# Optimization experiments

Measured on AMD Instinct MI355X. Metric: run time of the kernel, lower is better.

Reference implementation:

```python
import jax, jax.numpy as jnp
import numpy as np
from jax import lax

EPS = 1e-10
BN_EPS = 1e-5
T = 0.1
K = 64
B, D, H, Z = 2048, 2048, 512, 500


def _bn(x, g, b):
    # training-mode BatchNorm1d: biased batch stats over axis 0
    mu = x.mean(axis=0)
    var = ((x - mu) ** 2).mean(axis=0)
    return g * (x - mu) / jnp.sqrt(var + BN_EPS) + b


def _leaky(x):
    return jnp.where(x >= 0, x, 0.01 * x)


def setup_inputs() -> dict:
    key = jax.random.key(0)
    ks = jax.random.split(key, 16)
    def lin(k, fan_in, shape):
        return jax.random.normal(k, shape, jnp.float32) / np.sqrt(fan_in)
    return {
        'x': jax.random.uniform(ks[0], (B, D), jnp.float32),
        'u_gumbel': jax.random.uniform(ks[1], (B, D), jnp.float32),
        'eps': jax.random.normal(ks[2], (B, Z), jnp.float32),
        'wc_w1': lin(ks[3], D, (D, H)), 'wc_b1': jnp.zeros((H,)),
        'wc_g': jnp.ones((H,)), 'wc_beta': jnp.zeros((H,)),
        'wc_w2': lin(ks[4], H, (H, D)), 'wc_b2': jnp.zeros((D,)),
        'enc_w1': lin(ks[5], D, (D, 2 * H)), 'enc_b1': jnp.zeros((2 * H,)),
        'enc_g1': jnp.ones((2 * H,)), 'enc_beta1': jnp.zeros((2 * H,)),
        'enc_w2': lin(ks[6], 2 * H, (2 * H, H)), 'enc_b2': jnp.zeros((H,)),
        'enc_g2': jnp.ones((H,)), 'enc_beta2': jnp.zeros((H,)),
        'enc_w3': lin(ks[7], H, (H, H)), 'enc_b3': jnp.zeros((H,)),
        'enc_g3': jnp.ones((H,)), 'enc_beta3': jnp.zeros((H,)),
        'fc21_w': lin(ks[8], H, (H, Z)), 'fc21_b': jnp.zeros((Z,)),
        'fc22_w': lin(ks[9], H, (H, Z)), 'fc22_b': jnp.zeros((Z,)),
        'fc3_w': lin(ks[10], Z, (Z, H)), 'fc3_b': jnp.zeros((H,)),
        'fc3_g': jnp.ones((H,)), 'fc3_beta': jnp.zeros((H,)),
        'fc4_w': lin(ks[11], H, (H, D)), 'fc4_b': jnp.zeros((D,)),
    }


def _sample_subset(w_logits, u):
    # gumbel_keys: w += log(-log(u')) with u' in (EPS, 1)
    u = (1.0 - EPS) * u + EPS
    w = w_logits + jnp.log(-jnp.log(u))

    def step(carry, _):
        w, onehot, acc = carry
        khot_mask = jnp.maximum(1.0 - onehot, EPS)
        w = w + jnp.log(khot_mask)
        onehot = jax.nn.softmax(w / T, axis=-1)
        return (w, onehot, acc + onehot), None

    init = (w, jnp.zeros_like(w), jnp.zeros_like(w))
    (_, _, khot), _ = lax.scan(step, init, None, length=K)
    return khot


def reference(x, u_gumbel, eps,
              wc_w1, wc_b1, wc_g, wc_beta, wc_w2, wc_b2,
              enc_w1, enc_b1, enc_g1, enc_beta1,
              enc_w2, enc_b2, enc_g2, enc_beta2,
              enc_w3, enc_b3, enc_g3, enc_beta3,
              fc21_w, fc21_b, fc22_w, fc22_b,
              fc3_w, fc3_b, fc3_g, fc3_beta, fc4_w, fc4_b):
    # weight_creator: Linear -> BN -> ReLU -> Linear
    h = jax.nn.relu(_bn(x @ wc_w1 + wc_b1, wc_g, wc_beta))
    w_logits = h @ wc_w2 + wc_b2
    khot = _sample_subset(w_logits, u_gumbel)  # [B, D]
    xm = x * khot
    h1 = _leaky(_bn(xm @ enc_w1 + enc_b1, enc_g1, enc_beta1))
    h1 = _leaky(_bn(h1 @ enc_w2 + enc_b2, enc_g2, enc_beta2))
    h1 = _leaky(_bn(h1 @ enc_w3 + enc_b3, enc_g3, enc_beta3))
    mu = h1 @ fc21_w + fc21_b
    logvar = h1 @ fc22_w + fc22_b
    z = mu + eps * jnp.exp(0.5 * logvar)
    hd = _leaky(_bn(z @ fc3_w + fc3_b, fc3_g, fc3_beta))
    mu_x = jax.nn.sigmoid(hd @ fc4_w + fc4_b)
    return (mu_x, mu, logvar)
```

## Files before the change

kernel.cpp:

```cpp
#include <hip/hip_runtime.h>
#include <hip/hip_bf16.h>
#include <math.h>

#define B_DIM 2048
#define D_DIM 2048
#define H_DIM 512
#define Z_DIM 500

#define ACT_NONE 0
#define ACT_RELU 1
#define ACT_SIGMOID 2
#define ACT_LEAKY 3

typedef __attribute__((ext_vector_type(8))) _Float16 f16x8;
typedef __attribute__((ext_vector_type(4))) _Float16 f16x4;
typedef __attribute__((ext_vector_type(4))) float f32x4;

struct HL { _Float16 h, l; };
__device__ __forceinline__ HL split_f16(float a) {
    HL r;
    r.h = (_Float16)a;
    r.l = (_Float16)(a - (float)r.h);
    return r;
}

template<int TERMS>
__global__ __launch_bounds__(256, 2) void gemm_k(
    const float* __restrict__ A, const float* __restrict__ W,
    const float* __restrict__ bias, float* __restrict__ C,
    float* __restrict__ part, int M, int N, int K, int act, int Kc)
{
    constexpr int BM = 64, BN = 64, LDK = 40;
    constexpr int PS = BM * LDK;
    constexpr int NP = (TERMS == 3) ? 4 : 2;
    __shared__ _Float16 smem[2 * NP * PS];

    const int t = threadIdx.x;
    const int lane = t & 63;
    const int wv = t >> 6;
    const int wrow = wv >> 1, wcol = wv & 1;
    const int row0 = blockIdx.y * BM, col0 = blockIdx.x * BN;
    const int s = blockIdx.z;
    const int ks = s * Kc;
    const int ke = min(ks + Kc, K);
    const int nk = (ke > ks) ? ((ke - ks + 31) >> 5) : 0;

    const int ar = t >> 3;
    const int ako = (t & 7) << 2;
    const int bn_ = t & 63;
    const int bks = (t >> 6) << 3;
    const int gn = col0 + bn_;

    float4 aR[2];
    float bR[8];

    auto gload = [&](int kt) {
        int gk = kt + ako;
        #pragma unroll
        for (int p = 0; p < 2; ++p) {
            const float* ap = A + (size_t)(row0 + p * 32 + ar) * K + gk;
            float4 v = make_float4(0.f, 0.f, 0.f, 0.f);
            if (gk + 3 < ke) {
                v = *(const float4*)ap;
            } else {
                if (gk     < ke) v.x = ap[0];
                if (gk + 1 < ke) v.y = ap[1];
                if (gk + 2 < ke) v.z = ap[2];
                if (gk + 3 < ke) v.w = ap[3];
            }
            aR[p] = v;
        }
        #pragma unroll
        for (int i = 0; i < 8; ++i) {
            int gk2 = kt + bks + i;
            bR[i] = (gk2 < ke && gn < N) ? W[(size_t)gk2 * N + gn] : 0.f;
        }
    };

    auto cstore = [&](int b) {
        _Float16* Ah = smem + b * NP * PS;
        _Float16* Al = Ah + PS;
        _Float16* Bh = Ah + ((TERMS == 3) ? 2 : 1) * PS;
        _Float16* Bl = Bh + PS;
        #pragma unroll
        for (int p = 0; p < 2; ++p) {
            int r = p * 32 + ar;
            float4 v = aR[p];
            if constexpr (TERMS == 3) {
                HL s0 = split_f16(v.x), s1 = split_f16(v.y);
                HL s2 = split_f16(v.z), s3 = split_f16(v.w);
                f16x4 h4 = {s0.h, s1.h, s2.h, s3.h};
                f16x4 l4 = {s0.l, s1.l, s2.l, s3.l};
                *(f16x4*)&Ah[r * LDK + ako] = h4;
                *(f16x4*)&Al[r * LDK + ako] = l4;
            } else {
                f16x4 h4 = {(_Float16)v.x, (_Float16)v.y, (_Float16)v.z, (_Float16)v.w};
                *(f16x4*)&Ah[r * LDK + ako] = h4;
            }
        }
        if constexpr (TERMS == 3) {
            f16x8 h8, l8;
            #pragma unroll
            for (int i = 0; i < 8; ++i) { HL sp = split_f16(bR[i]); h8[i] = sp.h; l8[i] = sp.l; }
            *(f16x8*)&Bh[bn_ * LDK + bks] = h8;
            *(f16x8*)&Bl[bn_ * LDK + bks] = l8;
        } else {
            f16x8 h8;
            #pragma unroll
            for (int i = 0; i < 8; ++i) h8[i] = (_Float16)bR[i];
            *(f16x8*)&Bh[bn_ * LDK + bks] = h8;
        }
    };

    f32x4 acc[2][2];
    #pragma unroll
    for (int i = 0; i < 2; ++i)
        #pragma unroll
        for (int j = 0; j < 2; ++j) {
            f32x4 z = {0.f, 0.f, 0.f, 0.f};
            acc[i][j] = z;
        }

    const int q8 = (lane >> 4) * 8;
    const int fr = lane & 15;

    gload(ks);
    cstore(0);
    __syncthreads();

    for (int it = 0; it < nk; ++it) {
        int cur = it & 1;
        if (it + 1 < nk) gload(ks + (it + 1) * 32);

        {
            const _Float16* Ah = smem + cur * NP * PS;
            const _Float16* Al = Ah + PS;
            const _Float16* Bh = Ah + ((TERMS == 3) ? 2 : 1) * PS;
            const _Float16* Bl = Bh + PS;
            f16x8 ah[2], al[2], bh[2], bl[2];
            #pragma unroll
            for (int i = 0; i < 2; ++i) {
                int r = wrow * 32 + i * 16 + fr;
                ah[i] = *(const f16x8*)&Ah[r * LDK + q8];
                if constexpr (TERMS == 3) al[i] = *(const f16x8*)&Al[r * LDK + q8];
            }
            #pragma unroll
            for (int j = 0; j < 2; ++j) {
                int n = wcol * 32 + j * 16 + fr;
                bh[j] = *(const f16x8*)&Bh[n * LDK + q8];
                if constexpr (TERMS == 3) bl[j] = *(const f16x8*)&Bl[n * LDK + q8];
            }
            #pragma unroll
            for (int i = 0; i < 2; ++i)
                #pragma unroll
                for (int j = 0; j < 2; ++j) {
                    acc[i][j] = __builtin_amdgcn_mfma_f32_16x16x32_f16(ah[i], bh[j], acc[i][j], 0, 0, 0);
                    if constexpr (TERMS == 3) {
                        acc[i][j] = __builtin_amdgcn_mfma_f32_16x16x32_f16(ah[i], bl[j], acc[i][j], 0, 0, 0);
                        acc[i][j] = __builtin_amdgcn_mfma_f32_16x16x32_f16(al[i], bh[j], acc[i][j], 0, 0, 0);
                    }
                }
        }

        if (it + 1 < nk) cstore(cur ^ 1);
        __syncthreads();
    }

    const bool dopart = (gridDim.z > 1);
    float* dst = dopart ? (part + (size_t)s * M * N) : C;
    #pragma unroll
    for (int i = 0; i < 2; ++i) {
        int rbase = row0 + wrow * 32 + i * 16 + (lane >> 4) * 4;
        #pragma unroll
        for (int j = 0; j < 2; ++j) {
            int c = col0 + wcol * 32 + j * 16 + (lane & 15);
            if (c < N) {
                float b = dopart ? 0.f : bias[c];
                #pragma unroll
                for (int q = 0; q < 4; ++q) {
                    float v = acc[i][j][q] + b;
                    if (!dopart && act == ACT_SIGMOID)
                        v = 1.f / (1.f + __builtin_amdgcn_exp2f(-v * 1.44269504f));
                    dst[(size_t)(rbase + q) * N + c] = v;
                }
            }
        }
    }
}

__global__ __launch_bounds__(256) void reduce_bias(
    const float* __restrict__ part, int S, int MN, int N,
    const float* __restrict__ bias, float* __restrict__ C)
{
    int i = blockIdx.x * 256 + threadIdx.x;
    if (i >= MN) return;
    float s = bias[i % N];
    for (int k = 0; k < S; ++k) s += part[(size_t)k * MN + i];
    C[i] = s;
}

__global__ __launch_bounds__(256) void colstats_partial(
    const float* __restrict__ Y, float* __restrict__ part,
    int Brows, int N, int rowsPerBlock)
{
    const int t = threadIdx.x;
    const int col = blockIdx.x * 64 + (t & 63);
    const int g = blockIdx.y;
    const int r0 = g * rowsPerBlock;
    const int r1 = min(r0 + rowsPerBlock, Brows);
    float s = 0.f, s2 = 0.f;
    for (int r = r0 + (t >> 6); r < r1; r += 4) {
        float v = Y[(size_t)r * N + col];
        s += v;
        s2 += v * v;
    }
    __shared__ float ss[4][64], ss2[4][64];
    ss[t >> 6][t & 63] = s;
    ss2[t >> 6][t & 63] = s2;
    __syncthreads();
    if (t < 64) {
        s  = ss[0][t] + ss[1][t] + ss[2][t] + ss[3][t];
        s2 = ss2[0][t] + ss2[1][t] + ss2[2][t] + ss2[3][t];
        float* p = part + ((size_t)g * N + col) * 2;
        p[0] = s;
        p[1] = s2;
    }
}

__global__ __launch_bounds__(256) void colstats_final(
    const float* __restrict__ part, int G, int N, int Brows,
    const float* __restrict__ gamma, const float* __restrict__ beta,
    float* __restrict__ scale, float* __restrict__ shift)
{
    int c = blockIdx.x * 256 + threadIdx.x;
    if (c >= N) return;
    float s = 0.f, s2 = 0.f;
    for (int g = 0; g < G; ++g) {
        s  += part[((size_t)g * N + c) * 2];
        s2 += part[((size_t)g * N + c) * 2 + 1];
    }
    float invB = 1.f / (float)Brows;
    float mean = s * invB;
    float var  = s2 * invB - mean * mean;
    float rstd = rsqrtf(var + 1e-5f);
    float sc = gamma[c] * rstd;
    scale[c] = sc;
    shift[c] = beta[c] - mean * sc;
}

__global__ __launch_bounds__(256) void bn_apply(
    const float* __restrict__ Y, const float* __restrict__ scale,
    const float* __restrict__ shift, float* __restrict__ out,
    int total, int N, int act)
{
    int i4 = (blockIdx.x * 256 + threadIdx.x) * 4;
    if (i4 >= total) return;
    float4 y = *(const float4*)(Y + i4);
    int c = i4 % N;
    float4 sc = *(const float4*)(scale + c);
    float4 sh = *(const float4*)(shift + c);
    float4 r;
    r.x = y.x * sc.x + sh.x;
    r.y = y.y * sc.y + sh.y;
    r.z = y.z * sc.z + sh.z;
    r.w = y.w * sc.w + sh.w;
    if (act == ACT_RELU) {
        r.x = fmaxf(r.x, 0.f); r.y = fmaxf(r.y, 0.f);
        r.z = fmaxf(r.z, 0.f); r.w = fmaxf(r.w, 0.f);
    } else if (act == ACT_LEAKY) {
        r.x = (r.x >= 0.f) ? r.x : 0.01f * r.x;
        r.y = (r.y >= 0.f) ? r.y : 0.01f * r.y;
        r.z = (r.z >= 0.f) ? r.z : 0.01f * r.z;
        r.w = (r.w >= 0.f) ? r.w : 0.01f * r.w;
    }
    *(float4*)(out + i4) = r;
}

__global__ __launch_bounds__(256) void gumbel_scan_kernel(
    float* __restrict__ WL, const float* __restrict__ U,
    const float* __restrict__ X)
{
    const int row = blockIdx.x;
    const int t = threadIdx.x;
    const int wv = t >> 6;
    const int lane = t & 63;
    float* wrow = WL + (size_t)row * D_DIM;
    const float* urow = U + (size_t)row * D_DIM;
    const float* xrow = X + (size_t)row * D_DIM;

    const float L2E = 1.4426950408889634f;
    const float LOG2LN2 = -0.5287663729448977f;
    const float C10 = 10.0f;

    __shared__ float smax[4], ssum[4];

    float w2[8], oh[8], acc[8];
    #pragma unroll
    for (int j = 0; j < 8; ++j) {
        int c = t + j * 256;
        float u = urow[c];
        u = (1.0f - 1e-10f) * u + 1e-10f;
        float tl = -__builtin_amdgcn_logf(u);
        w2[j] = fmaf(wrow[c], L2E, __builtin_amdgcn_logf(tl) + LOG2LN2);
        oh[j] = 0.f;
        acc[j] = 0.f;
    }

    for (int it = 0; it < 64; ++it) {
        float m = -INFINITY;
        #pragma unroll
        for (int j = 0; j < 8; ++j) {
            float mask = fmaxf(1.0f - oh[j], 1e-10f);
            w2[j] += __builtin_amdgcn_logf(mask);
            m = fmaxf(m, w2[j]);
        }
        #pragma unroll
        for (int off = 32; off; off >>= 1)
            m = fmaxf(m, __shfl_xor(m, off));
        if (lane == 0) smax[wv] = m;
        __syncthreads();
        m = fmaxf(fmaxf(smax[0], smax[1]), fmaxf(smax[2], smax[3]));
        float mc = m * C10;
        float s = 0.f;
        #pragma unroll
        for (int j = 0; j < 8; ++j) {
            float e = __builtin_amdgcn_exp2f(fmaf(w2[j], C10, -mc));
            oh[j] = e;
            s += e;
        }
        #pragma unroll
        for (int off = 32; off; off >>= 1)
            s += __shfl_xor(s, off);
        if (lane == 0) ssum[wv] = s;
        __syncthreads();
        s = (ssum[0] + ssum[1]) + (ssum[2] + ssum[3]);
        float inv = 1.0f / s;
        #pragma unroll
        for (int j = 0; j < 8; ++j) {
            oh[j] *= inv;
            acc[j] += oh[j];
        }
    }

    #pragma unroll
    for (int j = 0; j < 8; ++j) {
        int c = t + j * 256;
        wrow[c] = xrow[c] * acc[j];
    }
}

__global__ __launch_bounds__(256) void z_kernel(
    const float* __restrict__ mu, const float* __restrict__ lv,
    const float* __restrict__ eps, float* __restrict__ z, int n4)
{
    int i = blockIdx.x * 256 + threadIdx.x;
    if (i >= n4) return;
    float4 m = ((const float4*)mu)[i];
    float4 l = ((const float4*)lv)[i];
    float4 e = ((const float4*)eps)[i];
    const float HL2E = 0.7213475204444817f;
    float4 r;
    r.x = m.x + e.x * __builtin_amdgcn_exp2f(l.x * HL2E);
    r.y = m.y + e.y * __builtin_amdgcn_exp2f(l.y * HL2E);
    r.z = m.z + e.z * __builtin_amdgcn_exp2f(l.z * HL2E);
    r.w = m.w + e.w * __builtin_amdgcn_exp2f(l.w * HL2E);
    ((float4*)z)[i] = r;
}

extern "C" void kernel_launch(void* const* d_in, const int* in_sizes, int n_in,
                              void* d_out, int out_size, void* d_ws, size_t ws_size,
                              hipStream_t stream) {
    const float* x        = (const float*)d_in[0];
    const float* u_gumbel = (const float*)d_in[1];
    const float* eps      = (const float*)d_in[2];
    const float* wc_w1    = (const float*)d_in[3];
    const float* wc_b1    = (const float*)d_in[4];
    const float* wc_g     = (const float*)d_in[5];
    const float* wc_beta  = (const float*)d_in[6];
    const float* wc_w2    = (const float*)d_in[7];
    const float* wc_b2    = (const float*)d_in[8];
    const float* enc_w1   = (const float*)d_in[9];
    const float* enc_b1   = (const float*)d_in[10];
    const float* enc_g1   = (const float*)d_in[11];
    const float* enc_beta1= (const float*)d_in[12];
    const float* enc_w2   = (const float*)d_in[13];
    const float* enc_b2   = (const float*)d_in[14];
    const float* enc_g2   = (const float*)d_in[15];
    const float* enc_beta2= (const float*)d_in[16];
    const float* enc_w3   = (const float*)d_in[17];
    const float* enc_b3   = (const float*)d_in[18];
    const float* enc_g3   = (const float*)d_in[19];
    const float* enc_beta3= (const float*)d_in[20];
    const float* fc21_w   = (const float*)d_in[21];
    const float* fc21_b   = (const float*)d_in[22];
    const float* fc22_w   = (const float*)d_in[23];
    const float* fc22_b   = (const float*)d_in[24];
    const float* fc3_w    = (const float*)d_in[25];
    const float* fc3_b    = (const float*)d_in[26];
    const float* fc3_g    = (const float*)d_in[27];
    const float* fc3_beta = (const float*)d_in[28];
    const float* fc4_w    = (const float*)d_in[29];
    const float* fc4_b    = (const float*)d_in[30];

    float* out   = (float*)d_out;
    float* mu_x  = out;
    float* mu    = out + (size_t)B_DIM * D_DIM;
    float* lv    = mu + (size_t)B_DIM * Z_DIM;

    const size_t M1 = 1048576;
    float* wsf   = (float*)d_ws;
    float* WL    = wsf;
    float* P     = wsf + 4 * M1;
    float* Hbuf  = wsf + 8 * M1;
    float* bnp   = wsf + 9 * M1;
    float* scale = bnp + 16384;
    float* shift = scale + 2048;

    float* Y2 = WL;
    float* Y3 = WL + 2 * M1;
    float* Y4 = WL + 3 * M1;
    float* Zb = WL;
    float* Y5 = WL + 1 * M1;

    const int G = 8;

    auto gemm = [&](int TERMS, const float* A, const float* W, const float* b,
                    float* C, float* part, int M, int N, int K, int act, int SK) {
        int Kc = ((K / SK + 31) / 32) * 32;
        dim3 grid((N + 63) / 64, M / 64, SK);
        if (TERMS == 3)
            gemm_k<3><<<grid, 256, 0, stream>>>(A, W, b, C, part, M, N, K, act, Kc);
        else
            gemm_k<1><<<grid, 256, 0, stream>>>(A, W, b, C, part, M, N, K, act, Kc);
    };
    auto reduceK = [&](const float* part, int S, int MN, int N, const float* b, float* C) {
        reduce_bias<<<(MN + 255) / 256, 256, 0, stream>>>(part, S, MN, N, b, C);
    };
    auto bn = [&](float* Y, const float* g_, const float* b_, int N, int act) {
        dim3 gp(N / 64, G);
        colstats_partial<<<gp, 256, 0, stream>>>(Y, bnp, B_DIM, N, B_DIM / G);
        colstats_final<<<(N + 255) / 256, 256, 0, stream>>>(bnp, G, N, B_DIM, g_, b_, scale, shift);
        int total = B_DIM * N;
        bn_apply<<<(total / 4 + 255) / 256, 256, 0, stream>>>(Y, scale, shift, Y, total, N, act);
    };

    gemm(3, x, wc_w1, nullptr, nullptr, P, B_DIM, H_DIM, D_DIM, ACT_NONE, 4);
    reduceK(P, 4, B_DIM * H_DIM, H_DIM, wc_b1, Hbuf);
    bn(Hbuf, wc_g, wc_beta, H_DIM, ACT_RELU);
    gemm(3, Hbuf, wc_w2, wc_b2, WL, nullptr, B_DIM, D_DIM, H_DIM, ACT_NONE, 1);

    gumbel_scan_kernel<<<B_DIM, 256, 0, stream>>>(WL, u_gumbel, x);

    gemm(1, WL, enc_w1, nullptr, nullptr, P, B_DIM, 2 * H_DIM, D_DIM, ACT_NONE, 2);
    reduceK(P, 2, B_DIM * 2 * H_DIM, 2 * H_DIM, enc_b1, Y2);
    bn(Y2, enc_g1, enc_beta1, 2 * H_DIM, ACT_LEAKY);
    gemm(1, Y2, enc_w2, nullptr, nullptr, P, B_DIM, H_DIM, 2 * H_DIM, ACT_NONE, 4);
    reduceK(P, 4, B_DIM * H_DIM, H_DIM, enc_b2, Y3);
    bn(Y3, enc_g2, enc_beta2, H_DIM, ACT_LEAKY);
    gemm(1, Y3, enc_w3, nullptr, nullptr, P, B_DIM, H_DIM, H_DIM, ACT_NONE, 4);
    reduceK(P, 4, B_DIM * H_DIM, H_DIM, enc_b3, Y4);
    bn(Y4, enc_g3, enc_beta3, H_DIM, ACT_LEAKY);

    gemm(1, Y4, fc21_w, nullptr, nullptr, P, B_DIM, Z_DIM, H_DIM, ACT_NONE, 4);
    reduceK(P, 4, B_DIM * Z_DIM, Z_DIM, fc21_b, mu);
    gemm(1, Y4, fc22_w, nullptr, nullptr, P, B_DIM, Z_DIM, H_DIM, ACT_NONE, 4);
    reduceK(P, 4, B_DIM * Z_DIM, Z_DIM, fc22_b, lv);

    int n4 = B_DIM * Z_DIM / 4;
    z_kernel<<<(n4 + 255) / 256, 256, 0, stream>>>(mu, lv, eps, Zb, n4);

    gemm(1, Zb, fc3_w, nullptr, nullptr, P, B_DIM, H_DIM, Z_DIM, ACT_NONE, 4);
    reduceK(P, 4, B_DIM * H_DIM, H_DIM, fc3_b, Y5);
    bn(Y5, fc3_g, fc3_beta, H_DIM, ACT_LEAKY);
    gemm(1, Y5, fc4_w, fc4_b, mu_x, nullptr, B_DIM, D_DIM, H_DIM, ACT_SIGMOID, 1);
}
```

Measured before the change: 473.7 us.

## Pre-convert activations and weights to fp16 transposed, retile GEMMs, rework gumbel scan

Inputs and weights are now converted once into fp16 (hi/lo split where three-term precision is needed), and weights are transposed to K-major so the GEMM loads f16x8 vectors directly instead of converting fp32 inside the kernel. The GEMM becomes a templated 128x64 tile. BN apply and the z kernel now write fp16 activations for the next layer. The gumbel top-k scan is reformulated in the linear domain with power-of-ten softmax terms and double-buffered shared reductions. The cost is extra conversion kernels each call and reduced precision in intermediate activations.

```diff
diff --git a/kernel.cpp b/kernel.cpp
--- a/kernel.cpp
+++ b/kernel.cpp
@@ -16,113 +16,76 @@
 typedef __attribute__((ext_vector_type(4))) _Float16 f16x4;
 typedef __attribute__((ext_vector_type(4))) float f32x4;
 
-struct HL { _Float16 h, l; };
-__device__ __forceinline__ HL split_f16(float a) {
-    HL r;
-    r.h = (_Float16)a;
-    r.l = (_Float16)(a - (float)r.h);
-    return r;
-}
-
-template<int TERMS>
-__global__ __launch_bounds__(256, 2) void gemm_k(
-    const float* __restrict__ A, const float* __restrict__ W,
+template<int BM, int BN, int TERMS>
+__global__ __launch_bounds__(256, 2) void gemm_f16(
+    const _Float16* __restrict__ Ah_, const _Float16* __restrict__ Al_,
+    const _Float16* __restrict__ Bh_, const _Float16* __restrict__ Bl_,
     const float* __restrict__ bias, float* __restrict__ C,
     float* __restrict__ part, int M, int N, int K, int act, int Kc)
 {
-    constexpr int BM = 64, BN = 64, LDK = 40;
-    constexpr int PS = BM * LDK;
-    constexpr int NP = (TERMS == 3) ? 4 : 2;
-    __shared__ _Float16 smem[2 * NP * PS];
-
-    const int t = threadIdx.x;
-    const int lane = t & 63;
-    const int wv = t >> 6;
+    constexpr int LDK = 40;
+    constexpr int NPL = (TERMS == 3) ? 2 : 1;
+    constexpr int PSA = BM * LDK, PSB = BN * LDK;
+    constexpr int BUF = NPL * (PSA + PSB);
+    constexpr int MT = BM / 32, NT = BN / 32;
+    constexpr int CA = BM / 64, CB = BN / 64;
+    __shared__ _Float16 smem[2 * BUF];
+
+    const int t = threadIdx.x, lane = t & 63, wv = t >> 6;
     const int wrow = wv >> 1, wcol = wv & 1;
     const int row0 = blockIdx.y * BM, col0 = blockIdx.x * BN;
-    const int s = blockIdx.z;
-    const int ks = s * Kc;
-    const int ke = min(ks + Kc, K);
-    const int nk = (ke > ks) ? ((ke - ks + 31) >> 5) : 0;
-
-    const int ar = t >> 3;
-    const int ako = (t & 7) << 2;
-    const int bn_ = t & 63;
-    const int bks = (t >> 6) << 3;
-    const int gn = col0 + bn_;
-
-    float4 aR[2];
-    float bR[8];
+    const int ks = blockIdx.z * Kc;
+    const int nk = Kc >> 5;
+
+    f16x8 rA[CA][NPL], rB[CB][NPL];
 
     auto gload = [&](int kt) {
-        int gk = kt + ako;
-        #pragma unroll
-        for (int p = 0; p < 2; ++p) {
-            const float* ap = A + (size_t)(row0 + p * 32 + ar) * K + gk;
-            float4 v = make_float4(0.f, 0.f, 0.f, 0.f);
-            if (gk + 3 < ke) {
-                v = *(const float4*)ap;
-            } else {
-                if (gk     < ke) v.x = ap[0];
-                if (gk + 1 < ke) v.y = ap[1];
-                if (gk + 2 < ke) v.z = ap[2];
-                if (gk + 3 < ke) v.w = ap[3];
-            }
-            aR[p] = v;
-        }
-        #pragma unroll
-        for (int i = 0; i < 8; ++i) {
-            int gk2 = kt + bks + i;
-            bR[i] = (gk2 < ke && gn < N) ? W[(size_t)gk2 * N + gn] : 0.f;
-        }
-    };
-
+        #pragma unroll
+        for (int i = 0; i < CA; ++i) {
+            int id = t + i * 256;
+            int r = id >> 2, ko = (id & 3) * 8;
+            size_t off = (size_t)(row0 + r) * K + kt + ko;
+            rA[i][0] = *(const f16x8*)(Ah_ + off);
+            if constexpr (TERMS == 3) rA[i][1] = *(const f16x8*)(Al_ + off);
+        }
+        #pragma unroll
+        for (int i = 0; i < CB; ++i) {
+            int id = t + i * 256;
+            int r = id >> 2, ko = (id & 3) * 8;
+            size_t off = (size_t)(col0 + r) * K + kt + ko;
+            rB[i][0] = *(const f16x8*)(Bh_ + off);
+            if constexpr (TERMS == 3) rB[i][1] = *(const f16x8*)(Bl_ + off);
+        }
+    };
     auto cstore = [&](int b) {
-        _Float16* Ah = smem + b * NP * PS;
-        _Float16* Al = Ah + PS;
-        _Float16* Bh = Ah + ((TERMS == 3) ? 2 : 1) * PS;
-        _Float16* Bl = Bh + PS;
-        #pragma unroll
-        for (int p = 0; p < 2; ++p) {
-            int r = p * 32 + ar;
-            float4 v = aR[p];
-            if constexpr (TERMS == 3) {
-                HL s0 = split_f16(v.x), s1 = split_f16(v.y);
-                HL s2 = split_f16(v.z), s3 = split_f16(v.w);
-                f16x4 h4 = {s0.h, s1.h, s2.h, s3.h};
-                f16x4 l4 = {s0.l, s1.l, s2.l, s3.l};
-                *(f16x4*)&Ah[r * LDK + ako] = h4;
-                *(f16x4*)&Al[r * LDK + ako] = l4;
-            } else {
-                f16x4 h4 = {(_Float16)v.x, (_Float16)v.y, (_Float16)v.z, (_Float16)v.w};
-                *(f16x4*)&Ah[r * LDK + ako] = h4;
-            }
-        }
-        if constexpr (TERMS == 3) {
-            f16x8 h8, l8;
-            #pragma unroll
-            for (int i = 0; i < 8; ++i) { HL sp = split_f16(bR[i]); h8[i] = sp.h; l8[i] = sp.l; }
-            *(f16x8*)&Bh[bn_ * LDK + bks] = h8;
-            *(f16x8*)&Bl[bn_ * LDK + bks] = l8;
-        } else {
-            f16x8 h8;
-            #pragma unroll
-            for (int i = 0; i < 8; ++i) h8[i] = (_Float16)bR[i];
-            *(f16x8*)&Bh[bn_ * LDK + bks] = h8;
-        }
-    };
-
-    f32x4 acc[2][2];
-    #pragma unroll
-    for (int i = 0; i < 2; ++i)
-        #pragma unroll
-        for (int j = 0; j < 2; ++j) {
+        _Float16* base = smem + b * BUF;
+        #pragma unroll
+        for (int i = 0; i < CA; ++i) {
+            int id = t + i * 256;
+            int r = id >> 2, ko = (id & 3) * 8;
+            *(f16x8*)&base[r * LDK + ko] = rA[i][0];
+            if constexpr (TERMS == 3) *(f16x8*)&base[PSA + r * LDK + ko] = rA[i][1];
+        }
+        _Float16* bb = base + NPL * PSA;
+        #pragma unroll
+        for (int i = 0; i < CB; ++i) {
+            int id = t + i * 256;
+            int r = id >> 2, ko = (id & 3) * 8;
+            *(f16x8*)&bb[r * LDK + ko] = rB[i][0];
+            if constexpr (TERMS == 3) *(f16x8*)&bb[PSB + r * LDK + ko] = rB[i][1];
+        }
+    };
+
+    f32x4 acc[MT][NT];
+    #pragma unroll
+    for (int i = 0; i < MT; ++i)
+        #pragma unroll
+        for (int j = 0; j < NT; ++j) {
             f32x4 z = {0.f, 0.f, 0.f, 0.f};
             acc[i][j] = z;
         }
 
-    const int q8 = (lane >> 4) * 8;
-    const int fr = lane & 15;
+    const int q8 = (lane >> 4) * 8, fr = lane & 15;
 
     gload(ks);
     cstore(0);
@@ -132,48 +95,46 @@
         int cur = it & 1;
         if (it + 1 < nk) gload(ks + (it + 1) * 32);
 
-        {
-            const _Float16* Ah = smem + cur * NP * PS;
-            const _Float16* Al = Ah + PS;
-            const _Float16* Bh = Ah + ((TERMS == 3) ? 2 : 1) * PS;
-            const _Float16* Bl = Bh + PS;
-            f16x8 ah[2], al[2], bh[2], bl[2];
+        const _Float16* A0 = smem + cur * BUF;
+        const _Float16* A1 = A0 + PSA;
+        const _Float16* B0 = A0 + NPL * PSA;
+        const _Float16* B1 = B0 + PSB;
+        f16x8 ah[MT], al[MT], bh[NT], bl[NT];
+        #pragma unroll
+        for (int i = 0; i < MT; ++i) {
+            int r = wrow * (BM / 2) + i * 16 + fr;
+            ah[i] = *(const f16x8*)&A0[r * LDK + q8];
+            if constexpr (TERMS == 3) al[i] = *(const f16x8*)&A1[r * LDK + q8];
+        }
+        #pragma unroll
+        for (int j = 0; j < NT; ++j) {
+            int n = wcol * (BN / 2) + j * 16 + fr;
+            bh[j] = *(const f16x8*)&B0[n * LDK + q8];
+            if constexpr (TERMS == 3) bl[j] = *(const f16x8*)&B1[n * LDK + q8];
+        }
+        #pragma unroll
+        for (int i = 0; i < MT; ++i)
             #pragma unroll
-            for (int i = 0; i < 2; ++i) {
-                int r = wrow * 32 + i * 16 + fr;
-                ah[i] = *(const f16x8*)&Ah[r * LDK + q8];
-                if constexpr (TERMS == 3) al[i] = *(const f16x8*)&Al[r * LDK + q8];
+            for (int j = 0; j < NT; ++j) {
+                acc[i][j] = __builtin_amdgcn_mfma_f32_16x16x32_f16(ah[i], bh[j], acc[i][j], 0, 0, 0);
+                if constexpr (TERMS == 3) {
+                    acc[i][j] = __builtin_amdgcn_mfma_f32_16x16x32_f16(ah[i], bl[j], acc[i][j], 0, 0, 0);
+                    acc[i][j] = __builtin_amdgcn_mfma_f32_16x16x32_f16(al[i], bh[j], acc[i][j], 0, 0, 0);
+                }
             }
-            #pragma unroll
-            for (int j = 0; j < 2; ++j) {
-                int n = wcol * 32 + j * 16 + fr;
-                bh[j] = *(const f16x8*)&Bh[n * LDK + q8];
-                if constexpr (TERMS == 3) bl[j] = *(const f16x8*)&Bl[n * LDK + q8];
-            }
-            #pragma unroll
-            for (int i = 0; i < 2; ++i)
-                #pragma unroll
-                for (int j = 0; j < 2; ++j) {
-                    acc[i][j] = __builtin_amdgcn_mfma_f32_16x16x32_f16(ah[i], bh[j], acc[i][j], 0, 0, 0);
-                    if constexpr (TERMS == 3) {
-                        acc[i][j] = __builtin_amdgcn_mfma_f32_16x16x32_f16(ah[i], bl[j], acc[i][j], 0, 0, 0);
-                        acc[i][j] = __builtin_amdgcn_mfma_f32_16x16x32_f16(al[i], bh[j], acc[i][j], 0, 0, 0);
-                    }
-                }
-        }
 
         if (it + 1 < nk) cstore(cur ^ 1);
         __syncthreads();
     }
 
     const bool dopart = (gridDim.z > 1);
-    float* dst = dopart ? (part + (size_t)s * M * N) : C;
-    #pragma unroll
-    for (int i = 0; i < 2; ++i) {
-        int rbase = row0 + wrow * 32 + i * 16 + (lane >> 4) * 4;
-        #pragma unroll
-        for (int j = 0; j < 2; ++j) {
-            int c = col0 + wcol * 32 + j * 16 + (lane & 15);
+    float* dst = dopart ? (part + (size_t)blockIdx.z * M * N) : C;
+    #pragma unroll
+    for (int i = 0; i < MT; ++i) {
+        int rbase = row0 + wrow * (BM / 2) + i * 16 + (lane >> 4) * 4;
+        #pragma unroll
+        for (int j = 0; j < NT; ++j) {
+            int c = col0 + wcol * (BN / 2) + j * 16 + (lane & 15);
             if (c < N) {
                 float b = dopart ? 0.f : bias[c];
                 #pragma unroll
@@ -188,14 +149,55 @@
     }
 }
 
+__global__ __launch_bounds__(256) void cvt_split_x(
+    const float* __restrict__ x, _Float16* __restrict__ xh,
+    _Float16* __restrict__ xl, int n4)
+{
+    int i = blockIdx.x * 256 + threadIdx.x;
+    if (i >= n4) return;
+    float4 v = ((const float4*)x)[i];
+    f16x4 h, l;
+    h[0]=(_Float16)v.x; l[0]=(_Float16)(v.x-(float)h[0]);
+    h[1]=(_Float16)v.y; l[1]=(_Float16)(v.y-(float)h[1]);
+    h[2]=(_Float16)v.z; l[2]=(_Float16)(v.z-(float)h[2]);
+    h[3]=(_Float16)v.w; l[3]=(_Float16)(v.w-(float)h[3]);
+    ((f16x4*)xh)[i] = h;
+    ((f16x4*)xl)[i] = l;
+}
+
+__global__ __launch_bounds__(256) void cvt_w_t(
+    const float* __restrict__ in, _Float16* __restrict__ outh,
+    _Float16* __restrict__ outl, int K, int N, int Kp)
+{
+    __shared__ float tile[32][33];
+    const int t = threadIdx.x;
+    const int tk0 = blockIdx.x * 32, tn0 = blockIdx.y * 32;
+    const int lx = t & 31, ly = t >> 5;
+    #pragma unroll
+    for (int r = 0; r < 4; ++r) {
+        int k = tk0 + ly + r * 8, n = tn0 + lx;
+        tile[ly + r * 8][lx] = (k < K && n < N) ? in[(size_t)k * N + n] : 0.f;
+    }
+    __syncthreads();
+    #pragma unroll
+    for (int r = 0; r < 4; ++r) {
+        int n = tn0 + ly + r * 8, k = tk0 + lx;
+        float v = tile[lx][ly + r * 8];
+        _Float16 h = (_Float16)v;
+        outh[(size_t)n * Kp + k] = h;
+        if (outl) outl[(size_t)n * Kp + k] = (_Float16)(v - (float)h);
+    }
+}
+
 __global__ __launch_bounds__(256) void reduce_bias(
     const float* __restrict__ part, int S, int MN, int N,
-    const float* __restrict__ bias, float* __restrict__ C)
+    const float* __restrict__ bias, float* __restrict__ C, int act)
 {
     int i = blockIdx.x * 256 + threadIdx.x;
     if (i >= MN) return;
     float s = bias[i % N];
     for (int k = 0; k < S; ++k) s += part[(size_t)k * MN + i];
+    if (act == ACT_SIGMOID) s = 1.f / (1.f + __builtin_amdgcn_exp2f(-s * 1.44269504f));
     C[i] = s;
 }
 
@@ -248,123 +250,132 @@
     shift[c] = beta[c] - mean * sc;
 }
 
-__global__ __launch_bounds__(256) void bn_apply(
+__global__ __launch_bounds__(256) void bn_apply_f16(
     const float* __restrict__ Y, const float* __restrict__ scale,
-    const float* __restrict__ shift, float* __restrict__ out,
-    int total, int N, int act)
-{
-    int i4 = (blockIdx.x * 256 + threadIdx.x) * 4;
+    const float* __restrict__ shift, _Float16* __restrict__ oh,
+    _Float16* __restrict__ ol, int total, int N, int act)
+{
+    int idx = blockIdx.x * 256 + threadIdx.x;
+    int i4 = idx * 4;
     if (i4 >= total) return;
     float4 y = *(const float4*)(Y + i4);
     int c = i4 % N;
     float4 sc = *(const float4*)(scale + c);
     float4 sh = *(const float4*)(shift + c);
-    float4 r;
-    r.x = y.x * sc.x + sh.x;
-    r.y = y.y * sc.y + sh.y;
-    r.z = y.z * sc.z + sh.z;
-    r.w = y.w * sc.w + sh.w;
-    if (act == ACT_RELU) {
-        r.x = fmaxf(r.x, 0.f); r.y = fmaxf(r.y, 0.f);
-        r.z = fmaxf(r.z, 0.f); r.w = fmaxf(r.w, 0.f);
-    } else if (act == ACT_LEAKY) {
-        r.x = (r.x >= 0.f) ? r.x : 0.01f * r.x;
-        r.y = (r.y >= 0.f) ? r.y : 0.01f * r.y;
-        r.z = (r.z >= 0.f) ? r.z : 0.01f * r.z;
-        r.w = (r.w >= 0.f) ? r.w : 0.01f * r.w;
-    }
-    *(float4*)(out + i4) = r;
-}
-
-__global__ __launch_bounds__(256) void gumbel_scan_kernel(
-    float* __restrict__ WL, const float* __restrict__ U,
-    const float* __restrict__ X)
+    float r[4];
+    r[0] = y.x * sc.x + sh.x;
+    r[1] = y.y * sc.y + sh.y;
+    r[2] = y.z * sc.z + sh.z;
+    r[3] = y.w * sc.w + sh.w;
+    #pragma unroll
+    for (int q = 0; q < 4; ++q) {
+        if (act == ACT_RELU) r[q] = fmaxf(r[q], 0.f);
+        else if (act == ACT_LEAKY) r[q] = (r[q] >= 0.f) ? r[q] : 0.01f * r[q];
+    }
+    f16x4 h;
+    #pragma unroll
+    for (int q = 0; q < 4; ++q) h[q] = (_Float16)r[q];
+    ((f16x4*)oh)[idx] = h;
+    if (ol) {
+        f16x4 l;
+        #pragma unroll
+        for (int q = 0; q < 4; ++q) l[q] = (_Float16)(r[q] - (float)h[q]);
+        ((f16x4*)ol)[idx] = l;
+    }
+}
+
+__global__ __launch_bounds__(256) void gumbel_scan(
+    const float* __restrict__ WLg, const float* __restrict__ U,
+    const float* __restrict__ X, _Float16* __restrict__ XM)
 {
     const int row = blockIdx.x;
-    const int t = threadIdx.x;
-    const int wv = t >> 6;
-    const int lane = t & 63;
-    float* wrow = WL + (size_t)row * D_DIM;
+    const int t = threadIdx.x, wv = t >> 6, lane = t & 63;
+    const float* wrow = WLg + (size_t)row * D_DIM;
     const float* urow = U + (size_t)row * D_DIM;
     const float* xrow = X + (size_t)row * D_DIM;
+    _Float16* xmrow = XM + (size_t)row * D_DIM;
 
     const float L2E = 1.4426950408889634f;
     const float LOG2LN2 = -0.5287663729448977f;
-    const float C10 = 10.0f;
-
-    __shared__ float smax[4], ssum[4];
-
-    float w2[8], oh[8], acc[8];
+
+    __shared__ float sW[2][4], sS[2][4];
+
+    float W[8], e[8], acc[8];
     #pragma unroll
     for (int j = 0; j < 8; ++j) {
         int c = t + j * 256;
-        float u = urow[c];
-        u = (1.0f - 1e-10f) * u + 1e-10f;
+        float u = fmaf(urow[c], 1.0f - 1e-10f, 1e-10f);
         float tl = -__builtin_amdgcn_logf(u);
-        w2[j] = fmaf(wrow[c], L2E, __builtin_amdgcn_logf(tl) + LOG2LN2);
-        oh[j] = 0.f;
+        float w2 = fmaf(wrow[c], L2E, __builtin_amdgcn_logf(tl) + LOG2LN2);
+        W[j] = __builtin_amdgcn_exp2f(w2);
+        e[j] = 0.f;
         acc[j] = 0.f;
     }
+    float inv = 0.f;
 
     for (int it = 0; it < 64; ++it) {
-        float m = -INFINITY;
+        const int p = it & 1;
+        float lm = 0.f;
         #pragma unroll
         for (int j = 0; j < 8; ++j) {
-            float mask = fmaxf(1.0f - oh[j], 1e-10f);
-            w2[j] += __builtin_amdgcn_logf(mask);
-            m = fmaxf(m, w2[j]);
+            acc[j] = fmaf(e[j], inv, acc[j]);
+            float msk = fmaxf(fmaf(-e[j], inv, 1.0f), 1e-10f);
+            W[j] *= msk;
+            lm = fmaxf(lm, W[j]);
         }
         #pragma unroll
         for (int off = 32; off; off >>= 1)
-            m = fmaxf(m, __shfl_xor(m, off));
-        if (lane == 0) smax[wv] = m;
+            lm = fmaxf(lm, __shfl_xor(lm, off));
+        if (lane == 0) sW[p][wv] = lm;
         __syncthreads();
-        m = fmaxf(fmaxf(smax[0], smax[1]), fmaxf(smax[2], smax[3]));
-        float mc = m * C10;
+        float Wm = fmaxf(fmaxf(sW[p][0], sW[p][1]), fmaxf(sW[p][2], sW[p][3]));
+        float rm = 1.0f / Wm;
         float s = 0.f;
         #pragma unroll
         for (int j = 0; j < 8; ++j) {
-            float e = __builtin_amdgcn_exp2f(fmaf(w2[j], C10, -mc));
-            oh[j] = e;
-            s += e;
+            float r1 = W[j] * rm;
+            float r2 = r1 * r1;
+            float r4 = r2 * r2;
+            float r5 = r4 * r1;
+            float ee = r5 * r5;
+            e[j] = ee;
+            s += ee;
         }
         #pragma unroll
         for (int off = 32; off; off >>= 1)
             s += __shfl_xor(s, off);
-        if (lane == 0) ssum[wv] = s;
+        if (lane == 0) sS[p][wv] = s;
         __syncthreads();
-        s = (ssum[0] + ssum[1]) + (ssum[2] + ssum[3]);
-        float inv = 1.0f / s;
-        #pragma unroll
-        for (int j = 0; j < 8; ++j) {
-            oh[j] *= inv;
-            acc[j] += oh[j];
-        }
+        s = (sS[p][0] + sS[p][1]) + (sS[p][2] + sS[p][3]);
+        inv = 1.0f / s;
     }
 
     #pragma unroll
     for (int j = 0; j < 8; ++j) {
         int c = t + j * 256;
-        wrow[c] = xrow[c] * acc[j];
-    }
-}
-
-__global__ __launch_bounds__(256) void z_kernel(
+        float a = fmaf(e[j], inv, acc[j]);
+        xmrow[c] = (_Float16)(xrow[c] * a);
+    }
+}
+
+__global__ __launch_bounds__(256) void z_kernel16(
     const float* __restrict__ mu, const float* __restrict__ lv,
-    const float* __restrict__ eps, float* __restrict__ z, int n4)
+    const float* __restrict__ eps, _Float16* __restrict__ zb, int n4)
 {
     int i = blockIdx.x * 256 + threadIdx.x;
     if (i >= n4) return;
-    float4 m = ((const float4*)mu)[i];
-    float4 l = ((const float4*)lv)[i];
-    float4 e = ((const float4*)eps)[i];
+    int f = i * 4;
+    int row = f / Z_DIM, col = f - row * Z_DIM;
+    float4 m = *(const float4*)(mu + f);
+    float4 l = *(const float4*)(lv + f);
+    float4 e = *(const float4*)(eps + f);
     const float HL2E = 0.7213475204444817f;
-    float4 r;
-    r.x = m.x + e.x * __builtin_amdgcn_exp2f(l.x * HL2E);
-    r.y = m.y + e.y * __builtin_amdgcn_exp2f(l.y * HL2E);
-    r.z = m.z + e.z * __builtin_amdgcn_exp2f(l.z * HL2E);
-    r.w = m.w + e.w * __builtin_amdgcn_exp2f(l.w * HL2E);
-    ((float4*)z)[i] = r;
+    f16x4 r;
+    r[0] = (_Float16)(m.x + e.x * __builtin_amdgcn_exp2f(l.x * HL2E));
+    r[1] = (_Float16)(m.y + e.y * __builtin_amdgcn_exp2f(l.y * HL2E));
+    r[2] = (_Float16)(m.z + e.z * __builtin_amdgcn_exp2f(l.z * HL2E));
+    r[3] = (_Float16)(m.w + e.w * __builtin_amdgcn_exp2f(l.w * HL2E));
+    *(f16x4*)(zb + (size_t)row * 512 + col) = r;
 }
 
 extern "C" void kernel_launch(void* const* d_in, const int* in_sizes, int n_in,
@@ -407,70 +418,109 @@
     float* mu    = out + (size_t)B_DIM * D_DIM;
     float* lv    = mu + (size_t)B_DIM * Z_DIM;
 
-    const size_t M1 = 1048576;
-    float* wsf   = (float*)d_ws;
-    float* WL    = wsf;
-    float* P     = wsf + 4 * M1;
-    float* Hbuf  = wsf + 8 * M1;
-    float* bnp   = wsf + 9 * M1;
-    float* scale = bnp + 16384;
-    float* shift = scale + 2048;
-
-    float* Y2 = WL;
-    float* Y3 = WL + 2 * M1;
-    float* Y4 = WL + 3 * M1;
-    float* Zb = WL;
-    float* Y5 = WL + 1 * M1;
+    const size_t F1M = 1u << 20;
+    float* wsf = (float*)d_ws;
+    float*     P_WL  = wsf;
+    _Float16*  xh    = (_Float16*)(wsf + 4 * F1M);
+    _Float16*  xl    = (_Float16*)(wsf + 6 * F1M);
+    _Float16*  xm16  = (_Float16*)(wsf + 4 * F1M);
+    float*     Yb    = wsf + 6 * F1M;
+    _Float16*  a2    = (_Float16*)(wsf + 8 * F1M);
+    _Float16*  a3    = (_Float16*)(wsf + 9 * F1M);
+    _Float16*  a4    = (_Float16*)(wsf + 9 * F1M + F1M / 2);
+    _Float16*  zb16  = (_Float16*)(wsf + 10 * F1M);
+    _Float16*  a5    = (_Float16*)(wsf + 10 * F1M + F1M / 2);
+    float*     Hbuf  = wsf + 11 * F1M;
+    _Float16*  Hh    = (_Float16*)(wsf + 12 * F1M);
+    _Float16*  Hl    = (_Float16*)(wsf + 12 * F1M + F1M / 2);
+    _Float16*  w1th  = (_Float16*)(wsf + 13 * F1M);
+    _Float16*  w1tl  = (_Float16*)(wsf + 13 * F1M + F1M / 2);
+    _Float16*  w2th  = (_Float16*)(wsf + 14 * F1M);
+    _Float16*  w2tl  = (_Float16*)(wsf + 14 * F1M + F1M / 2);
+    _Float16*  e1t   = (_Float16*)(wsf + 15 * F1M);
+    _Float16*  e2t   = (_Float16*)(wsf + 16 * F1M);
+    _Float16*  e3t   = (_Float16*)(wsf + 16 * F1M + F1M / 4);
+    _Float16*  f21t  = (_Float16*)(wsf + 16 * F1M + 3 * (F1M / 8));
+    _Float16*  f22t  = (_Float16*)(wsf + 16 * F1M + 4 * (F1M / 8));
+    _Float16*  f3t   = (_Float16*)(wsf + 16 * F1M + 5 * (F1M / 8));
+    _Float16*  f4t   = (_Float16*)(wsf + 16 * F1M + 6 * (F1M / 8));
+    float*     bnp   = wsf + 17 * F1M + F1M / 4;
+    float*     scale = bnp + 16384;
+    float*     shift = scale + 2048;
 
     const int G = 8;
 
-    auto gemm = [&](int TERMS, const float* A, const float* W, const float* b,
-                    float* C, float* part, int M, int N, int K, int act, int SK) {
-        int Kc = ((K / SK + 31) / 32) * 32;
-        dim3 grid((N + 63) / 64, M / 64, SK);
-        if (TERMS == 3)
-            gemm_k<3><<<grid, 256, 0, stream>>>(A, W, b, C, part, M, N, K, act, Kc);
-        else
-            gemm_k<1><<<grid, 256, 0, stream>>>(A, W, b, C, part, M, N, K, act, Kc);
-    };
-    auto reduceK = [&](const float* part, int S, int MN, int N, const float* b, float* C) {
-        reduce_bias<<<(MN + 255) / 256, 256, 0, stream>>>(part, S, MN, N, b, C);
-    };
-    auto bn = [&](float* Y, const float* g_, const float* b_, int N, int act) {
+    auto gemm3 = [&](const _Float16* Ah, const _Float16* Al,
+                     const _Float16* Bh, const _Float16* Bl,
+                     const float* b, float* C, float* part,
+                     int N, int K, int SK) {
+        dim3 grid((N + 63) / 64, B_DIM / 128, SK);
+        gemm_f16<128, 64, 3><<<grid, 256, 0, stream>>>(Ah, Al, Bh, Bl, b, C, part,
+                                                       B_DIM, N, K, ACT_NONE, K / SK);
+    };
+    auto gemm1 = [&](const _Float16* Ah, const _Float16* Bh,
+                     const float* b, float* C, float* part,
+                     int N, int K, int act, int SK) {
+        dim3 grid((N + 63) / 64, B_DIM / 128, SK);
+        gemm_f16<128, 64, 1><<<grid, 256, 0, stream>>>(Ah, nullptr, Bh, nullptr, b, C,
+                                                       part, B_DIM, N, K, act, K / SK);
+    };
+    auto reduceK = [&](const float* part, int S, int N, const float* b, float* C) {
+        int MN = B_DIM * N;
+        reduce_bias<<<(MN + 255) / 256, 256, 0, stream>>>(part, S, MN, N, b, C, ACT_NONE);
+    };
+    auto bn = [&](const float* Y, const float* g_, const float* b_,
+                  _Float16* oh, _Float16* ol, int N, int act) {
         dim3 gp(N / 64, G);
         colstats_partial<<<gp, 256, 0, stream>>>(Y, bnp, B_DIM, N, B_DIM / G);
         colstats_final<<<(N + 255) / 256, 256, 0, stream>>>(bnp, G, N, B_DIM, g_, b_, scale, shift);
         int total = B_DIM * N;
-        bn_apply<<<(total / 4 + 255) / 256, 256, 0, stream>>>(Y, scale, shift, Y, total, N, act);
-    };
-
-    gemm(3, x, wc_w1, nullptr, nullptr, P, B_DIM, H_DIM, D_DIM, ACT_NONE, 4);
-    reduceK(P, 4, B_DIM * H_DIM, H_DIM, wc_b1, Hbuf);
-    bn(Hbuf, wc_g, wc_beta, H_DIM, ACT_RELU);
-    gemm(3, Hbuf, wc_w2, wc_b2, WL, nullptr, B_DIM, D_DIM, H_DIM, ACT_NONE, 1);
-
-    gumbel_scan_kernel<<<B_DIM, 256, 0, stream>>>(WL, u_gumbel, x);
-
-    gemm(1, WL, enc_w1, nullptr, nullptr, P, B_DIM, 2 * H_DIM, D_DIM, ACT_NONE, 2);
-    reduceK(P, 2, B_DIM * 2 * H_DIM, 2 * H_DIM, enc_b1, Y2);
-    bn(Y2, enc_g1, enc_beta1, 2 * H_DIM, ACT_LEAKY);
-    gemm(1, Y2, enc_w2, nullptr, nullptr, P, B_DIM, H_DIM, 2 * H_DIM, ACT_NONE, 4);
-    reduceK(P, 4, B_DIM * H_DIM, H_DIM, enc_b2, Y3);
-    bn(Y3, enc_g2, enc_beta2, H_DIM, ACT_LEAKY);
-    gemm(1, Y3, enc_w3, nullptr, nullptr, P, B_DIM, H_DIM, H_DIM, ACT_NONE, 4);
-    reduceK(P, 4, B_DIM * H_DIM, H_DIM, enc_b3, Y4);
-    bn(Y4, enc_g3, enc_beta3, H_DIM, ACT_LEAKY);
-
-    gemm(1, Y4, fc21_w, nullptr, nullptr, P, B_DIM, Z_DIM, H_DIM, ACT_NONE, 4);
-    reduceK(P, 4, B_DIM * Z_DIM, Z_DIM, fc21_b, mu);
-    gemm(1, Y4, fc22_w, nullptr, nullptr, P, B_DIM, Z_DIM, H_DIM, ACT_NONE, 4);
-    reduceK(P, 4, B_DIM * Z_DIM, Z_DIM, fc22_b, lv);
-
+        bn_apply_f16<<<(total / 4 + 255) / 256, 256, 0, stream>>>(Y, scale, shift, oh, ol, total, N, act);
+    };
+    auto cvtw = [&](const float* in, _Float16* oh, _Float16* ol, int K, int N, int Kp, int Np) {
+        dim3 grid(Kp / 32, Np / 32);
+        cvt_w_t<<<grid, 256, 0, stream>>>(in, oh, ol, K, N, Kp);
+    };
+
+    cvt_split_x<<<4096, 256, 0, stream>>>(x, xh, xl, B_DIM * D_DIM / 4);
+    cvtw(wc_w1, w1th, w1tl, 2048, 512, 2048, 512);
+    cvtw(wc_w2, w2th, w2tl, 512, 2048, 512, 2048);
+    cvtw(enc_w1, e1t, nullptr, 2048, 1024, 2048, 1024);
+    cvtw(enc_w2, e2t, nullptr, 1024, 512, 1024, 512);
+    cvtw(enc_w3, e3t, nullptr, 512, 512, 512, 512);
+    cvtw(fc21_w, f21t, nullptr, 512, 500, 512, 512);
+    cvtw(fc22_w, f22t, nullptr, 512, 500, 512, 512);
+    cvtw(fc3_w, f3t, nullptr, 500, 512, 512, 512);
+    cvtw(fc4_w, f4t, nullptr, 512, 2048, 512, 2048);
+
+    gemm3(xh, xl, w1th, w1tl, nullptr, nullptr, P_WL, 512, 2048, 4);
+    reduceK(P_WL, 4, 512, wc_b1, Hbuf);
+    bn(Hbuf, wc_g, wc_beta, Hh, Hl, 512, ACT_RELU);
+    gemm3(Hh, Hl, w2th, w2tl, wc_b2, P_WL, nullptr, 2048, 512, 1);
+
+    gumbel_scan<<<B_DIM, 256, 0, stream>>>(P_WL, u_gumbel, x, xm16);
+
+    gemm1(xm16, e1t, nullptr, nullptr, P_WL, 1024, 2048, ACT_NONE, 2);
+    reduceK(P_WL, 2, 1024, enc_b1, Yb);
+    bn(Yb, enc_g1, enc_beta1, a2, nullptr, 1024, ACT_LEAKY);
+    gemm1(a2, e2t, nullptr, nullptr, P_WL, 512, 1024, ACT_NONE, 4);
+    reduceK(P_WL, 4, 512, enc_b2, Yb);
+    bn(Yb, enc_g2, enc_beta2, a3, nullptr, 512, ACT_LEAKY);
+    gemm1(a3, e3t, nullptr, nullptr, P_WL, 512, 512, ACT_NONE, 4);
+    reduceK(P_WL, 4, 512, enc_b3, Yb);
+    bn(Yb, enc_g3, enc_beta3, a4, nullptr, 512, ACT_LEAKY);
+
+    gemm1(a4, f21t, nullptr, nullptr, P_WL, 500, 512, ACT_NONE, 4);
+    reduceK(P_WL, 4, 500, fc21_b, mu);
+    gemm1(a4, f22t, nullptr, nullptr, P_WL, 500, 512, ACT_NONE, 4);
+    reduceK(P_WL, 4, 500, fc22_b, lv);
+
+    hipMemsetAsync(zb16, 0, (size_t)B_DIM * 512 * sizeof(_Float16), stream);
     int n4 = B_DIM * Z_DIM / 4;
-    z_kernel<<<(n4 + 255) / 256, 256, 0, stream>>>(mu, lv, eps, Zb, n4);
-
-    gemm(1, Zb, fc3_w, nullptr, nullptr, P, B_DIM, H_DIM, Z_DIM, ACT_NONE, 4);
-    reduceK(P, 4, B_DIM * H_DIM, H_DIM, fc3_b, Y5);
-    bn(Y5, fc3_g, fc3_beta, H_DIM, ACT_LEAKY);
-    gemm(1, Y5, fc4_w, fc4_b, mu_x, nullptr, B_DIM, D_DIM, H_DIM, ACT_SIGMOID, 1);
-}
+    z_kernel16<<<(n4 + 255) / 256, 256, 0, stream>>>(mu, lv, eps, zb16, n4);
+
+    gemm1(zb16, f3t, nullptr, nullptr, P_WL, 512, 512, ACT_NONE, 4);
+    reduceK(P_WL, 4, 512, fc3_b, Yb);
+    bn(Yb, fc3_g, fc3_beta, a5, nullptr, 512, ACT_LEAKY);
+    gemm1(a5, f4t, fc4_b, mu_x, nullptr, 2048, 512, ACT_SIGMOID, 1);
+}
```

Result: no change. 465.2 us (-1.8%).
